# Performance work log

Hardware: AMD Instinct MI355X
Metric: run time of the kernel (lower is better)

Reference implementation:

```python
import jax, jax.numpy as jnp
import numpy as np

B, N1, N2, D, L, H = 2, 384, 384, 128, 3, 128
DM_MIN = 0.5


def _gat_layer(x, adj, W, Wb, A, gW, gb):
    # GAT_gate from jaechanglim/DTI_PDBbind: attention softmax over dim 1, gated residual
    h = x @ W + Wb                                   # [B,N,D]
    e = jnp.einsum('bjl,bkl->bjk', h @ A, h)
    e = e + jnp.swapaxes(e, 1, 2)
    att = jnp.where(adj > 0, e, -9e15)
    att = jax.nn.softmax(att, axis=1) * adj
    h_prime = jax.nn.relu(jnp.einsum('bij,bjk->bik', att, h))
    coeff = jax.nn.sigmoid(jnp.concatenate([x, h_prime], -1) @ gW + gb)  # [B,N,1]
    return coeff * x + (1.0 - coeff) * h_prime


def _pair_mlp(h1g, h2g, W1, b1, W2, b2):
    # MLP(concat(h1_i, h2_j)) without materializing the [B,N1,N2,2D] concat:
    # split W1 into ligand / protein halves and broadcast-add the projections.
    p1 = jnp.einsum('bnd,dk->bnk', h1g, W1[:D])      # [B,N1,H]
    p2 = jnp.einsum('bmd,dk->bmk', h2g, W1[D:])      # [B,N2,H]
    hid = jax.nn.relu(p1[:, :, None, :] + p2[:, None, :, :] + b1)  # [B,N1,N2,H]
    return (hid @ W2 + b2)[..., 0]                   # [B,N1,N2]


def reference(h1, adj1, h2, dmv, charge1, charge2, vdw_epsilon, vdw_sigma,
              delta_uff, valid1, valid2, no_metal1, no_metal2,
              node_W, gat_W, gat_Wb, gat_A, gat_gW, gat_gb,
              pair_W1, pair_b1, pair_W2, pair_b2,
              vdw_coeff, duff_coeff, int_W1, int_b1, int_W2, int_b2):
    h1g = h1 @ node_W
    h2g = h2 @ node_W
    for i in range(L):  # only ligand graph is convolved (as in the source)
        h1g = _gat_layer(h1g, adj1, gat_W[i], gat_Wb[i], gat_A[i], gat_gW[i], gat_gb[i])

    dm = jnp.sqrt(jnp.sum(dmv * dmv, -1) + 1e-10)    # [B,N1,N2]
    dm = jnp.where(dm < DM_MIN, 1e10, dm)

    # coulomb term (pair MLPs 0,1)
    cA = jax.nn.sigmoid(_pair_mlp(h1g, h2g, pair_W1[0], pair_b1[0], pair_W2[0], pair_b2[0]))
    cN = jax.nn.sigmoid(_pair_mlp(h1g, h2g, pair_W1[1], pair_b1[1], pair_W2[1], pair_b2[1])) * 2.0 + 1.0
    charge12 = charge1[:, :, None] * charge2[:, None, :]
    e_c = cA * charge12 * jnp.power(1.0 / dm, cN)
    e_c = e_c * valid1[:, :, None] * valid2[:, None, :]
    e_c = jnp.clip(e_c, -100.0, 100.0)
    e_c = jnp.sum(e_c, axis=(1, 2))[:, None]

    # vdw term (pair MLPs 2=A sigmoid, 3=B tanh, 4=N sigmoid)
    vA = (jax.nn.sigmoid(_pair_mlp(h1g, h2g, pair_W1[2], pair_b1[2], pair_W2[2], pair_b2[2])) * 0.6 + 0.7)
    vA = vA * (vdw_coeff[0] * vdw_coeff[0]) * vdw_epsilon
    vB = jnp.tanh(_pair_mlp(h1g, h2g, pair_W1[3], pair_b1[3], pair_W2[3], pair_b2[3])) * 0.6 + 0.7
    vN = jax.nn.sigmoid(_pair_mlp(h1g, h2g, pair_W1[4], pair_b1[4], pair_W2[4], pair_b2[4])) * 2.0 + 5.0
    dm0 = vdw_sigma * vB
    dm0 = jnp.where(dm0 < 1e-4, 1.0, dm0)
    r = jnp.power(dm0 / dm, vN)
    e_v = vA * (r * r - 2.0 * r)                     # (dm0/dm)^(2N) - 2(dm0/dm)^N
    e_v = e_v * no_metal1[:, :, None] * no_metal2[:, None, :]
    e_v = jnp.minimum(e_v, 100.0)
    e_v = jnp.sum(e_v, axis=(1, 2))[:, None]

    # conformational energy difference term
    e_u = (duff_coeff[0] * duff_coeff[0] * delta_uff)[:, None]

    # learned intercept from pooled ligand features
    hs = jnp.sum(h1g * valid1[..., None], axis=1)
    inter = jax.nn.relu(hs @ int_W1 + int_b1) @ int_W2 + int_b2

    return jnp.concatenate([e_c, e_v, e_u, inter], -1)  # [B,4]


def setup_inputs() -> dict:
    key = jax.random.key(0)
    ks = jax.random.split(key, 24)
    inp = {}
    inp['h1'] = jax.random.normal(ks[0], (B, N1, 54), jnp.float32)
    inp['h2'] = jax.random.normal(ks[1], (B, N2, 54), jnp.float32)
    a = jax.random.uniform(ks[2], (B, N1, N1))
    adj = (a > 0.9).astype(jnp.float32)
    adj = jnp.maximum(adj, jnp.swapaxes(adj, 1, 2))
    inp['adj1'] = jnp.maximum(adj, jnp.eye(N1, dtype=jnp.float32)[None])
    inp['dmv'] = jax.random.normal(ks[3], (B, N1, N2, 3), jnp.float32) * 3.0
    inp['charge1'] = jax.random.normal(ks[4], (B, N1), jnp.float32) * 0.3
    inp['charge2'] = jax.random.normal(ks[5], (B, N2), jnp.float32) * 0.3
    inp['vdw_epsilon'] = jax.random.uniform(ks[6], (B, N1, N2), jnp.float32) * 0.3
    inp['vdw_sigma'] = 3.0 + jax.random.uniform(ks[7], (B, N1, N2), jnp.float32)
    inp['delta_uff'] = jax.random.uniform(ks[8], (B,), jnp.float32) * 5.0
    inp['valid1'] = jnp.ones((B, N1), jnp.float32)
    inp['valid2'] = jnp.ones((B, N2), jnp.float32)
    inp['no_metal1'] = jnp.ones((B, N1), jnp.float32)
    inp['no_metal2'] = jnp.ones((B, N2), jnp.float32)
    # parameters
    inp['node_W'] = jax.random.normal(ks[9], (54, D), jnp.float32) * 0.1
    inp['gat_W'] = jax.random.normal(ks[10], (L, D, D), jnp.float32) * (1.0 / np.sqrt(D))
    inp['gat_Wb'] = jnp.zeros((L, D), jnp.float32)
    inp['gat_A'] = jax.random.normal(ks[11], (L, D, D), jnp.float32) * 0.05
    inp['gat_gW'] = jax.random.normal(ks[12], (L, 2 * D, 1), jnp.float32) * 0.05
    inp['gat_gb'] = jnp.zeros((L, 1), jnp.float32)
    inp['pair_W1'] = jax.random.normal(ks[13], (5, 2 * D, H), jnp.float32) * 0.05
    inp['pair_b1'] = jnp.zeros((5, H), jnp.float32)
    inp['pair_W2'] = jax.random.normal(ks[14], (5, H, 1), jnp.float32) * 0.1
    inp['pair_b2'] = jnp.zeros((5, 1), jnp.float32)
    inp['vdw_coeff'] = jnp.array([0.02], jnp.float32)
    inp['duff_coeff'] = jnp.array([0.1], jnp.float32)
    inp['int_W1'] = jax.random.normal(ks[15], (D, H), jnp.float32) * 0.05
    inp['int_b1'] = jnp.zeros((H,), jnp.float32)
    inp['int_W2'] = jax.random.normal(ks[16], (H, 1), jnp.float32) * 0.1
    inp['int_b2'] = jnp.zeros((1,), jnp.float32)
    return inp
```

## Files before the change

### kernel.cpp

```cpp
#include <hip/hip_runtime.h>
#include <math.h>

#define BB 2
#define NN 384
#define DD 128
#define HH 128
#define RT_ALL (BB * NN)
#define PCOLS (BB * NN)

__device__ __forceinline__ float sigmoidf_(float x) { return 1.f / (1.f + __expf(-x)); }
__device__ __forceinline__ float tanhf_(float x)    { return 1.f - 2.f / (__expf(2.f * x) + 1.f); }

__global__ __launch_bounds__(256) void k_embed(
    const float* __restrict__ h1, const float* __restrict__ h2,
    const float* __restrict__ nW, float* __restrict__ h1g, float* __restrict__ h2g) {
  int r0 = blockIdx.x * 2;
  int tid = threadIdx.x;
  const float* src; float* dst; int rb;
  if (r0 < RT_ALL) { src = h1; dst = h1g; rb = r0; }
  else             { src = h2; dst = h2g; rb = r0 - RT_ALL; }
  __shared__ float xs[2][54];
  if (tid < 108) xs[tid / 54][tid % 54] = src[rb * 54 + tid];
  __syncthreads();
  int rr = tid >> 7, c = tid & 127;
  float acc = 0.f;
#pragma unroll 6
  for (int k = 0; k < 54; ++k) acc += xs[rr][k] * nW[k * DD + c];
  dst[(rb + rr) * DD + c] = acc;
}

__global__ __launch_bounds__(256) void k_gat_hhA(
    const float* __restrict__ x, const float* __restrict__ W,
    const float* __restrict__ Wb, const float* __restrict__ A,
    float* __restrict__ h, float* __restrict__ hA,
    float* __restrict__ hT, float* __restrict__ hAT) {
  int r = blockIdx.x;
  int tid = threadIdx.x, c = tid & 127, kh = tid >> 7;
  __shared__ float xs[DD], hs[DD];
  __shared__ float ph[2][DD];
  if (tid < DD) xs[tid] = x[r * DD + tid];
  __syncthreads();
  float acc = 0.f;
  const float* Wp = W + (kh * 64) * DD + c;
#pragma unroll 4
  for (int k = 0; k < 64; ++k) acc += xs[kh * 64 + k] * Wp[k * DD];
  ph[kh][c] = acc;
  __syncthreads();
  if (tid < DD) {
    float hv = ph[0][tid] + ph[1][tid] + Wb[tid];
    h[r * DD + tid] = hv; hT[tid * PCOLS + r] = hv; hs[tid] = hv;
  }
  __syncthreads();
  acc = 0.f;
  const float* Ap = A + (kh * 64) * DD + c;
#pragma unroll 4
  for (int k = 0; k < 64; ++k) acc += hs[kh * 64 + k] * Ap[k * DD];
  ph[kh][c] = acc;
  __syncthreads();
  if (tid < DD) {
    float av = ph[0][tid] + ph[1][tid];
    hA[r * DD + tid] = av; hAT[tid * PCOLS + r] = av;
  }
}

__global__ __launch_bounds__(384) void k_gat_att(
    const float* __restrict__ h, const float* __restrict__ hA,
    const float* __restrict__ hT, const float* __restrict__ hAT,
    const float* __restrict__ adj, float* __restrict__ att) {
  int col = blockIdx.x;
  int b = col / NN, k = col - b * NN;
  int tid = threadIdx.x;
  __shared__ float hrow_s[DD], hArow_s[DD];
  __shared__ float rmx[6], rsm[6];
  if (tid < DD) hrow_s[tid] = h[col * DD + tid];
  else if (tid < 2 * DD) hArow_s[tid - DD] = hA[col * DD + tid - DD];
  __syncthreads();
  const float* hTb  = hT  + b * NN + tid;
  const float* hATb = hAT + b * NN + tid;
  float e = 0.f;
#pragma unroll 8
  for (int c = 0; c < DD; ++c)
    e += hATb[c * PCOLS] * hrow_s[c] + hTb[c * PCOLS] * hArow_s[c];
  float a = adj[col * NN + tid];
  float lmax = (a > 0.f) ? e : -3e38f;
#pragma unroll
  for (int off = 32; off > 0; off >>= 1) lmax = fmaxf(lmax, __shfl_down(lmax, off));
  if ((tid & 63) == 0) rmx[tid >> 6] = lmax;
  __syncthreads();
  float m = fmaxf(fmaxf(fmaxf(rmx[0], rmx[1]), fmaxf(rmx[2], rmx[3])), fmaxf(rmx[4], rmx[5]));
  float v = (a > 0.f) ? __expf(e - m) : 0.f;
  float s = v;
#pragma unroll
  for (int off = 32; off > 0; off >>= 1) s += __shfl_down(s, off);
  if ((tid & 63) == 0) rsm[tid >> 6] = s;
  __syncthreads();
  float inv = 1.f / (rsm[0] + rsm[1] + rsm[2] + rsm[3] + rsm[4] + rsm[5]);
  att[(b * NN + tid) * NN + k] = v * a * inv;
}

__global__ __launch_bounds__(256) void k_gat_out(
    const float* __restrict__ x, const float* __restrict__ h,
    const float* __restrict__ att, const float* __restrict__ gW,
    const float* __restrict__ gb, float* __restrict__ out) {
  int r = blockIdx.x;
  int b = r / NN;
  int tid = threadIdx.x, c = tid & 127, jh = tid >> 7;
  __shared__ float arow[NN];
  __shared__ float ph[2][DD];
  __shared__ float redw[2];
  if (tid < 96) ((float4*)arow)[tid] = ((const float4*)(att + r * NN))[tid];
  __syncthreads();
  float accA = 0.f, accB = 0.f;
  const float* hp = h + (b * NN + jh * 192) * DD + c;
  const float* ar = arow + jh * 192;
#pragma unroll 4
  for (int jj = 0; jj < 192; jj += 2) {
    accA += ar[jj] * hp[jj * DD];
    accB += ar[jj + 1] * hp[(jj + 1) * DD];
  }
  ph[jh][c] = accA + accB;
  __syncthreads();
  if (tid < DD) {
    float hpr = fmaxf(ph[0][tid] + ph[1][tid], 0.f);
    float xr = x[r * DD + tid];
    float v = xr * gW[tid] + hpr * gW[DD + tid];
#pragma unroll
    for (int off = 32; off > 0; off >>= 1) v += __shfl_down(v, off);
    if ((tid & 63) == 0) redw[tid >> 6] = v;
  }
  __syncthreads();
  if (tid < DD) {
    float hpr = fmaxf(ph[0][tid] + ph[1][tid], 0.f);
    float xr = x[r * DD + tid];
    float coeff = sigmoidf_(redw[0] + redw[1] + gb[0]);
    out[r * DD + tid] = coeff * xr + (1.f - coeff) * hpr;
  }
}

__global__ __launch_bounds__(256) void k_pair_proj(
    const float* __restrict__ h1g, const float* __restrict__ h2g,
    const float* __restrict__ W1, const float* __restrict__ b1,
    const float* __restrict__ delta_uff, const float* __restrict__ duff_coeff,
    float* __restrict__ p1, float* __restrict__ p2q, float* __restrict__ out) {
  const int RT = 16;
  int m = blockIdx.x % 5;
  int r0 = (blockIdx.x / 5) * RT;
  int tid = threadIdx.x, c = tid & 127, kh = tid >> 7;
  if (blockIdx.x == 0 && tid < BB * 4) {
    int bb = tid >> 2, cc = tid & 3;
    out[tid] = (cc == 2) ? duff_coeff[0] * duff_coeff[0] * delta_uff[bb] : 0.f;
  }
  bool lig = (r0 < RT_ALL);
  const float* src = lig ? h1g : h2g;
  int rb = lig ? r0 : r0 - RT_ALL;
  const float* W = W1 + (m * 256 + (lig ? 0 : 128)) * HH;
  __shared__ float xs[RT][DD];
  __shared__ float ps[RT][DD];
  for (int idx = tid; idx < RT * DD; idx += 256) xs[idx >> 7][idx & 127] = src[rb * DD + idx];
  __syncthreads();
  float acc[RT];
#pragma unroll
  for (int r = 0; r < RT; ++r) acc[r] = 0.f;
  const float* Wp = W + (kh * 64) * HH + c;
#pragma unroll 2
  for (int k = 0; k < 64; ++k) {
    float w = Wp[k * HH];
#pragma unroll
    for (int r = 0; r < RT; ++r) acc[r] += xs[r][kh * 64 + k] * w;
  }
  if (kh == 1) {
#pragma unroll
    for (int r = 0; r < RT; ++r) ps[r][c] = acc[r];
  }
  __syncthreads();
  if (kh == 0) {
    if (lig) {
      float bias = b1[m * HH + c];
#pragma unroll
      for (int r = 0; r < RT; ++r)
        p1[((rb + r) * 5 + m) * HH + c] = acc[r] + ps[r][c] + bias;
    } else {
      int g = m * (HH / 4) + (c >> 2);
      float* dst = p2q + (size_t)(g * PCOLS + rb) * 4 + (c & 3);
#pragma unroll
      for (int r = 0; r < RT; ++r) dst[4 * r] = acc[r] + ps[r][c];
    }
  }
}

__global__ __launch_bounds__(192) void k_pair_energy(
    const float* __restrict__ p1, const float* __restrict__ p2q,
    const float* __restrict__ W2, const float* __restrict__ b2,
    const float* __restrict__ dmv, const float* __restrict__ charge1,
    const float* __restrict__ charge2, const float* __restrict__ veps,
    const float* __restrict__ vsig, const float* __restrict__ valid1,
    const float* __restrict__ valid2, const float* __restrict__ nm1,
    const float* __restrict__ nm2, const float* __restrict__ vdw_coeff,
    const float* __restrict__ h1g, float* __restrict__ ws_int,
    float* __restrict__ out) {
  int tid = threadIdx.x;
  if (blockIdx.x >= 768) {
    int eb = blockIdx.x - 768;
    int b = eb >> 2, ch = eb & 3;
    if (tid < DD) {
      float acc = 0.f;
      int i0 = ch * 96;
#pragma unroll 4
      for (int i = 0; i < 96; ++i) {
        int gi = b * NN + i0 + i;
        acc += h1g[gi * DD + tid] * valid1[gi];
      }
      ws_int[eb * DD + tid] = acc;
    }
    return;
  }
  const int TI = 2;
  int tile = blockIdx.x >> 1, jh = blockIdx.x & 1;
  int r0 = tile * TI;
  int b = r0 / NN;
  int j = jh * 192 + tid;
  int col = b * NN + j;

  __shared__ float4 p1s4[2][5 * HH / 4];
  __shared__ float4 w2s4[5 * HH / 4];
  {
    const float4* p1g = (const float4*)(p1 + r0 * 5 * HH);
    for (int idx = tid; idx < 2 * 160; idx += 192) p1s4[idx / 160][idx % 160] = p1g[idx];
    if (tid < 160) w2s4[tid] = ((const float4*)W2)[tid];
  }
  __syncthreads();

  const float4* p2q4 = (const float4*)p2q;
  float acc0[5], acc1[5];
#pragma unroll
  for (int m = 0; m < 5; ++m) {
    const float4* pc = p2q4 + (size_t)(m * 32) * PCOLS + col;
    float a0 = 0.f, a1 = 0.f;
#pragma unroll 8
    for (int hq = 0; hq < 32; ++hq) {
      float4 pv = pc[(size_t)hq * PCOLS];
      float4 x0 = p1s4[0][m * 32 + hq];
      float4 x1 = p1s4[1][m * 32 + hq];
      float4 w  = w2s4[m * 32 + hq];
      a0 += fmaxf(x0.x + pv.x, 0.f) * w.x + fmaxf(x0.y + pv.y, 0.f) * w.y
          + fmaxf(x0.z + pv.z, 0.f) * w.z + fmaxf(x0.w + pv.w, 0.f) * w.w;
      a1 += fmaxf(x1.x + pv.x, 0.f) * w.x + fmaxf(x1.y + pv.y, 0.f) * w.y
          + fmaxf(x1.z + pv.z, 0.f) * w.z + fmaxf(x1.w + pv.w, 0.f) * w.w;
    }
    acc0[m] = a0 + b2[m]; acc1[m] = a1 + b2[m];
  }

  float q2c = charge2[col], v2 = valid2[col], n2 = nm2[col];
  float vc2 = vdw_coeff[0] * vdw_coeff[0];
  float ec_sum = 0.f, ev_sum = 0.f;
#pragma unroll
  for (int ti = 0; ti < TI; ++ti) {
    const float* am = ti ? acc1 : acc0;
    int gi = r0 + ti;
    int pidx = gi * NN + j;
    float dx = dmv[pidx * 3 + 0], dy = dmv[pidx * 3 + 1], dz = dmv[pidx * 3 + 2];
    float dm = sqrtf(dx * dx + dy * dy + dz * dz + 1e-10f);
    if (dm < 0.5f) dm = 1e10f;
    float cA = sigmoidf_(am[0]);
    float cN = sigmoidf_(am[1]) * 2.f + 1.f;
    float e_c = cA * charge1[gi] * q2c * __powf(1.f / dm, cN);
    e_c *= valid1[gi] * v2;
    e_c = fminf(fmaxf(e_c, -100.f), 100.f);
    ec_sum += e_c;
    float vA = (sigmoidf_(am[2]) * 0.6f + 0.7f) * vc2 * veps[pidx];
    float vB = tanhf_(am[3]) * 0.6f + 0.7f;
    float vN = sigmoidf_(am[4]) * 2.f + 5.f;
    float dm0 = vsig[pidx] * vB;
    if (dm0 < 1e-4f) dm0 = 1.f;
    float rr = __powf(dm0 / dm, vN);
    float e_v = vA * (rr * rr - 2.f * rr);
    e_v *= nm1[gi] * n2;
    e_v = fminf(e_v, 100.f);
    ev_sum += e_v;
  }
#pragma unroll
  for (int off = 32; off > 0; off >>= 1) {
    ec_sum += __shfl_down(ec_sum, off);
    ev_sum += __shfl_down(ev_sum, off);
  }
  __shared__ float rec[3], rev[3];
  if ((tid & 63) == 0) { rec[tid >> 6] = ec_sum; rev[tid >> 6] = ev_sum; }
  __syncthreads();
  if (tid == 0) {
    atomicAdd(&out[b * 4 + 0], rec[0] + rec[1] + rec[2]);
    atomicAdd(&out[b * 4 + 1], rev[0] + rev[1] + rev[2]);
  }
}

__global__ __launch_bounds__(256) void k_intercept_fin(
    const float* __restrict__ ws_int, const float* __restrict__ W1,
    const float* __restrict__ b1, const float* __restrict__ W2,
    const float* __restrict__ b2, float* __restrict__ out) {
  int b = blockIdx.x;
  int tid = threadIdx.x, c = tid & 127, kh = tid >> 7;
  __shared__ float hsf[DD];
  __shared__ float ph[2][DD];
  __shared__ float redw[2];
  if (tid < DD)
    hsf[tid] = ws_int[(b * 4 + 0) * DD + tid] + ws_int[(b * 4 + 1) * DD + tid]
             + ws_int[(b * 4 + 2) * DD + tid] + ws_int[(b * 4 + 3) * DD + tid];
  __syncthreads();
  float acc = 0.f;
  const float* Wp = W1 + (kh * 64) * HH + c;
#pragma unroll 4
  for (int k = 0; k < 64; ++k) acc += hsf[kh * 64 + k] * Wp[k * HH];
  ph[kh][c] = acc;
  __syncthreads();
  if (tid < DD) {
    float hid = fmaxf(ph[0][tid] + ph[1][tid] + b1[tid], 0.f);
    float v = hid * W2[tid];
#pragma unroll
    for (int off = 32; off > 0; off >>= 1) v += __shfl_down(v, off);
    if ((tid & 63) == 0) redw[tid >> 6] = v;
  }
  __syncthreads();
  if (tid == 0) out[b * 4 + 3] = redw[0] + redw[1] + b2[0];
}

extern "C" void kernel_launch(void* const* d_in, const int* in_sizes, int n_in,
                              void* d_out, int out_size, void* d_ws, size_t ws_size,
                              hipStream_t stream) {
  (void)in_sizes; (void)n_in; (void)out_size; (void)ws_size;
  const float* h1         = (const float*)d_in[0];
  const float* h2         = (const float*)d_in[1];
  const float* adj1       = (const float*)d_in[2];
  const float* dmv        = (const float*)d_in[3];
  const float* charge1    = (const float*)d_in[4];
  const float* charge2    = (const float*)d_in[5];
  const float* veps       = (const float*)d_in[6];
  const float* vsig       = (const float*)d_in[7];
  const float* delta_uff  = (const float*)d_in[8];
  const float* valid1     = (const float*)d_in[9];
  const float* valid2     = (const float*)d_in[10];
  const float* nm1        = (const float*)d_in[11];
  const float* nm2        = (const float*)d_in[12];
  const float* node_W     = (const float*)d_in[13];
  const float* gat_W      = (const float*)d_in[14];
  const float* gat_Wb     = (const float*)d_in[15];
  const float* gat_A      = (const float*)d_in[16];
  const float* gat_gW     = (const float*)d_in[17];
  const float* gat_gb     = (const float*)d_in[18];
  const float* pW1        = (const float*)d_in[19];
  const float* pb1        = (const float*)d_in[20];
  const float* pW2        = (const float*)d_in[21];
  const float* pb2        = (const float*)d_in[22];
  const float* vdw_coeff  = (const float*)d_in[23];
  const float* duff_coeff = (const float*)d_in[24];
  const float* iW1        = (const float*)d_in[25];
  const float* ib1        = (const float*)d_in[26];
  const float* iW2        = (const float*)d_in[27];
  const float* ib2        = (const float*)d_in[28];
  float* out = (float*)d_out;

  float* ws = (float*)d_ws;
  const int RN = BB * NN * DD;
  float* h1gA   = ws;
  float* h1gB   = h1gA + RN;
  float* h2g    = h1gB + RN;
  float* hbuf   = h2g + RN;
  float* hAbuf  = hbuf + RN;
  float* hTbuf  = hAbuf + RN;
  float* hATbuf = hTbuf + RN;
  float* att    = hATbuf + RN;
  float* p1     = att + BB * NN * NN;
  float* p2q    = p1 + BB * NN * 5 * HH;
  float* ws_int = p2q + 5 * HH * PCOLS;

  k_embed<<<dim3(2 * BB * NN / 2), dim3(256), 0, stream>>>(h1, h2, node_W, h1gA, h2g);

  float* cur = h1gA;
  float* nxt = h1gB;
  for (int l = 0; l < 3; ++l) {
    k_gat_hhA<<<dim3(BB * NN), dim3(256), 0, stream>>>(
        cur, gat_W + l * DD * DD, gat_Wb + l * DD, gat_A + l * DD * DD,
        hbuf, hAbuf, hTbuf, hATbuf);
    k_gat_att<<<dim3(BB * NN), dim3(384), 0, stream>>>(
        hbuf, hAbuf, hTbuf, hATbuf, adj1, att);
    k_gat_out<<<dim3(BB * NN), dim3(256), 0, stream>>>(
        cur, hbuf, att, gat_gW + l * 2 * DD, gat_gb + l, nxt);
    float* t = cur; cur = nxt; nxt = t;
  }
  const float* h1gF = cur;

  k_pair_proj<<<dim3((2 * BB * NN / 16) * 5), dim3(256), 0, stream>>>(
      h1gF, h2g, pW1, pb1, delta_uff, duff_coeff, p1, p2q, out);
  k_pair_energy<<<dim3(768 + 8), dim3(192), 0, stream>>>(
      p1, p2q, pW2, pb2, dmv, charge1, charge2, veps, vsig,
      valid1, valid2, nm1, nm2, vdw_coeff, h1gF, ws_int, out);
  k_intercept_fin<<<dim3(BB), dim3(256), 0, stream>>>(ws_int, iW1, ib1, iW2, ib2, out);
}
```

Before: 316.2 us.

## Process two rows per block in GAT kernels and drop shared-memory staging

The GAT projection, attention and output kernels now each handle two rows or columns per block, so every weight or h load is reused for two outputs and the launch count is halved. Shared-memory staging of inputs is removed in several kernels in favour of direct global reads, which are uniform across the block and so can be served by scalar or broadcast loads. The pair-energy kernel switches to 384-thread blocks covering a full protein row, reading p1 and W2 from global instead of shared memory. This trades fewer blocks, and possibly lower occupancy, for more reuse per load, and relies on the cache to serve the repeated global reads.

```diff
diff --git a/kernel.cpp b/kernel.cpp
--- a/kernel.cpp
+++ b/kernel.cpp
@@ -19,13 +19,11 @@
   const float* src; float* dst; int rb;
   if (r0 < RT_ALL) { src = h1; dst = h1g; rb = r0; }
   else             { src = h2; dst = h2g; rb = r0 - RT_ALL; }
-  __shared__ float xs[2][54];
-  if (tid < 108) xs[tid / 54][tid % 54] = src[rb * 54 + tid];
-  __syncthreads();
   int rr = tid >> 7, c = tid & 127;
+  const float* xr = src + (rb + rr) * 54;
   float acc = 0.f;
 #pragma unroll 6
-  for (int k = 0; k < 54; ++k) acc += xs[rr][k] * nW[k * DD + c];
+  for (int k = 0; k < 54; ++k) acc += xr[k] * nW[k * DD + c];
   dst[(rb + rr) * DD + c] = acc;
 }
 
@@ -34,32 +32,46 @@
     const float* __restrict__ Wb, const float* __restrict__ A,
     float* __restrict__ h, float* __restrict__ hA,
     float* __restrict__ hT, float* __restrict__ hAT) {
-  int r = blockIdx.x;
+  int r0 = blockIdx.x * 2;
   int tid = threadIdx.x, c = tid & 127, kh = tid >> 7;
-  __shared__ float xs[DD], hs[DD];
-  __shared__ float ph[2][DD];
-  if (tid < DD) xs[tid] = x[r * DD + tid];
-  __syncthreads();
-  float acc = 0.f;
+  __shared__ float ph[2][2][DD];
+  __shared__ float hs[2][DD];
+  const float* x0 = x + (r0 + 0) * DD + kh * 64;
+  const float* x1 = x + (r0 + 1) * DD + kh * 64;
   const float* Wp = W + (kh * 64) * DD + c;
-#pragma unroll 4
-  for (int k = 0; k < 64; ++k) acc += xs[kh * 64 + k] * Wp[k * DD];
-  ph[kh][c] = acc;
-  __syncthreads();
-  if (tid < DD) {
-    float hv = ph[0][tid] + ph[1][tid] + Wb[tid];
-    h[r * DD + tid] = hv; hT[tid * PCOLS + r] = hv; hs[tid] = hv;
-  }
-  __syncthreads();
-  acc = 0.f;
+  float a00 = 0.f, a01 = 0.f, a10 = 0.f, a11 = 0.f;
+#pragma unroll 4
+  for (int k = 0; k < 64; k += 2) {
+    float w0 = Wp[k * DD], w1 = Wp[(k + 1) * DD];
+    a00 += x0[k] * w0; a01 += x0[k + 1] * w1;
+    a10 += x1[k] * w0; a11 += x1[k + 1] * w1;
+  }
+  ph[kh][0][c] = a00 + a01;
+  ph[kh][1][c] = a10 + a11;
+  __syncthreads();
+  {
+    float hv = ph[0][kh][c] + ph[1][kh][c] + Wb[c];
+    h[(r0 + kh) * DD + c] = hv;
+    hT[c * PCOLS + r0 + kh] = hv;
+    hs[kh][c] = hv;
+  }
+  __syncthreads();
   const float* Ap = A + (kh * 64) * DD + c;
-#pragma unroll 4
-  for (int k = 0; k < 64; ++k) acc += hs[kh * 64 + k] * Ap[k * DD];
-  ph[kh][c] = acc;
-  __syncthreads();
-  if (tid < DD) {
-    float av = ph[0][tid] + ph[1][tid];
-    hA[r * DD + tid] = av; hAT[tid * PCOLS + r] = av;
+  a00 = a01 = a10 = a11 = 0.f;
+#pragma unroll 4
+  for (int k = 0; k < 64; k += 2) {
+    float w0 = Ap[k * DD], w1 = Ap[(k + 1) * DD];
+    a00 += hs[0][kh * 64 + k] * w0; a01 += hs[0][kh * 64 + k + 1] * w1;
+    a10 += hs[1][kh * 64 + k] * w0; a11 += hs[1][kh * 64 + k + 1] * w1;
+  }
+  __syncthreads();
+  ph[kh][0][c] = a00 + a01;
+  ph[kh][1][c] = a10 + a11;
+  __syncthreads();
+  {
+    float av = ph[0][kh][c] + ph[1][kh][c];
+    hA[(r0 + kh) * DD + c] = av;
+    hAT[c * PCOLS + r0 + kh] = av;
   }
 }
 
@@ -67,74 +79,87 @@
     const float* __restrict__ h, const float* __restrict__ hA,
     const float* __restrict__ hT, const float* __restrict__ hAT,
     const float* __restrict__ adj, float* __restrict__ att) {
-  int col = blockIdx.x;
-  int b = col / NN, k = col - b * NN;
+  int b = blockIdx.x / (NN / 2);
+  int k0 = (blockIdx.x % (NN / 2)) * 2;
+  int col0 = b * NN + k0, col1 = col0 + 1;
   int tid = threadIdx.x;
-  __shared__ float hrow_s[DD], hArow_s[DD];
-  __shared__ float rmx[6], rsm[6];
-  if (tid < DD) hrow_s[tid] = h[col * DD + tid];
-  else if (tid < 2 * DD) hArow_s[tid - DD] = hA[col * DD + tid - DD];
-  __syncthreads();
+  const float* hr0  = h  + col0 * DD;
+  const float* har0 = hA + col0 * DD;
+  const float* hr1  = h  + col1 * DD;
+  const float* har1 = hA + col1 * DD;
   const float* hTb  = hT  + b * NN + tid;
   const float* hATb = hAT + b * NN + tid;
-  float e = 0.f;
-#pragma unroll 8
-  for (int c = 0; c < DD; ++c)
-    e += hATb[c * PCOLS] * hrow_s[c] + hTb[c * PCOLS] * hArow_s[c];
-  float a = adj[col * NN + tid];
-  float lmax = (a > 0.f) ? e : -3e38f;
-#pragma unroll
-  for (int off = 32; off > 0; off >>= 1) lmax = fmaxf(lmax, __shfl_down(lmax, off));
-  if ((tid & 63) == 0) rmx[tid >> 6] = lmax;
-  __syncthreads();
-  float m = fmaxf(fmaxf(fmaxf(rmx[0], rmx[1]), fmaxf(rmx[2], rmx[3])), fmaxf(rmx[4], rmx[5]));
-  float v = (a > 0.f) ? __expf(e - m) : 0.f;
-  float s = v;
-#pragma unroll
-  for (int off = 32; off > 0; off >>= 1) s += __shfl_down(s, off);
-  if ((tid & 63) == 0) rsm[tid >> 6] = s;
-  __syncthreads();
-  float inv = 1.f / (rsm[0] + rsm[1] + rsm[2] + rsm[3] + rsm[4] + rsm[5]);
-  att[(b * NN + tid) * NN + k] = v * a * inv;
+  float e0a = 0.f, e0b = 0.f, e1a = 0.f, e1b = 0.f;
+#pragma unroll 4
+  for (int c = 0; c < DD; ++c) {
+    float hTv = hTb[c * PCOLS], hATv = hATb[c * PCOLS];
+    e0a += hATv * hr0[c]; e0b += hTv * har0[c];
+    e1a += hATv * hr1[c]; e1b += hTv * har1[c];
+  }
+  float e0 = e0a + e0b, e1 = e1a + e1b;
+  float a0 = adj[col0 * NN + tid];
+  float a1 = adj[col1 * NN + tid];
+  __shared__ float rmx0[6], rmx1[6], rsm0[6], rsm1[6];
+  float l0 = (a0 > 0.f) ? e0 : -3e38f;
+  float l1 = (a1 > 0.f) ? e1 : -3e38f;
+#pragma unroll
+  for (int off = 32; off > 0; off >>= 1) {
+    l0 = fmaxf(l0, __shfl_down(l0, off));
+    l1 = fmaxf(l1, __shfl_down(l1, off));
+  }
+  if ((tid & 63) == 0) { rmx0[tid >> 6] = l0; rmx1[tid >> 6] = l1; }
+  __syncthreads();
+  float m0 = rmx0[0], m1 = rmx1[0];
+#pragma unroll
+  for (int w = 1; w < 6; ++w) { m0 = fmaxf(m0, rmx0[w]); m1 = fmaxf(m1, rmx1[w]); }
+  float v0 = (a0 > 0.f) ? __expf(e0 - m0) : 0.f;
+  float v1 = (a1 > 0.f) ? __expf(e1 - m1) : 0.f;
+  float s0 = v0, s1 = v1;
+#pragma unroll
+  for (int off = 32; off > 0; off >>= 1) {
+    s0 += __shfl_down(s0, off);
+    s1 += __shfl_down(s1, off);
+  }
+  if ((tid & 63) == 0) { rsm0[tid >> 6] = s0; rsm1[tid >> 6] = s1; }
+  __syncthreads();
+  float d0 = 0.f, d1 = 0.f;
+#pragma unroll
+  for (int w = 0; w < 6; ++w) { d0 += rsm0[w]; d1 += rsm1[w]; }
+  float2 wv = make_float2(v0 * a0 / d0, v1 * a1 / d1);
+  *(float2*)(att + (b * NN + tid) * NN + k0) = wv;
 }
 
 __global__ __launch_bounds__(256) void k_gat_out(
     const float* __restrict__ x, const float* __restrict__ h,
     const float* __restrict__ att, const float* __restrict__ gW,
     const float* __restrict__ gb, float* __restrict__ out) {
-  int r = blockIdx.x;
-  int b = r / NN;
+  int r0 = blockIdx.x * 2;
+  int b = r0 / NN;
   int tid = threadIdx.x, c = tid & 127, jh = tid >> 7;
-  __shared__ float arow[NN];
-  __shared__ float ph[2][DD];
-  __shared__ float redw[2];
-  if (tid < 96) ((float4*)arow)[tid] = ((const float4*)(att + r * NN))[tid];
-  __syncthreads();
-  float accA = 0.f, accB = 0.f;
+  __shared__ float ph[2][2][DD];
+  __shared__ float redw[2][2];
+  const float* ar0 = att + (r0 + 0) * NN + jh * 192;
+  const float* ar1 = att + (r0 + 1) * NN + jh * 192;
   const float* hp = h + (b * NN + jh * 192) * DD + c;
-  const float* ar = arow + jh * 192;
+  float a0A = 0.f, a0B = 0.f, a1A = 0.f, a1B = 0.f;
 #pragma unroll 4
   for (int jj = 0; jj < 192; jj += 2) {
-    accA += ar[jj] * hp[jj * DD];
-    accB += ar[jj + 1] * hp[(jj + 1) * DD];
-  }
-  ph[jh][c] = accA + accB;
-  __syncthreads();
-  if (tid < DD) {
-    float hpr = fmaxf(ph[0][tid] + ph[1][tid], 0.f);
-    float xr = x[r * DD + tid];
-    float v = xr * gW[tid] + hpr * gW[DD + tid];
-#pragma unroll
-    for (int off = 32; off > 0; off >>= 1) v += __shfl_down(v, off);
-    if ((tid & 63) == 0) redw[tid >> 6] = v;
-  }
-  __syncthreads();
-  if (tid < DD) {
-    float hpr = fmaxf(ph[0][tid] + ph[1][tid], 0.f);
-    float xr = x[r * DD + tid];
-    float coeff = sigmoidf_(redw[0] + redw[1] + gb[0]);
-    out[r * DD + tid] = coeff * xr + (1.f - coeff) * hpr;
-  }
+    float hv0 = hp[jj * DD], hv1 = hp[(jj + 1) * DD];
+    a0A += ar0[jj] * hv0; a0B += ar0[jj + 1] * hv1;
+    a1A += ar1[jj] * hv0; a1B += ar1[jj + 1] * hv1;
+  }
+  ph[jh][0][c] = a0A + a0B;
+  ph[jh][1][c] = a1A + a1B;
+  __syncthreads();
+  float hpr = fmaxf(ph[0][jh][c] + ph[1][jh][c], 0.f);
+  float xr = x[(r0 + jh) * DD + c];
+  float v = xr * gW[c] + hpr * gW[DD + c];
+#pragma unroll
+  for (int off = 32; off > 0; off >>= 1) v += __shfl_down(v, off);
+  if ((tid & 63) == 0) redw[jh][(tid >> 6) & 1] = v;
+  __syncthreads();
+  float coeff = sigmoidf_(redw[jh][0] + redw[jh][1] + gb[0]);
+  out[(r0 + jh) * DD + c] = coeff * xr + (1.f - coeff) * hpr;
 }
 
 __global__ __launch_bounds__(256) void k_pair_proj(
@@ -154,20 +179,18 @@
   const float* src = lig ? h1g : h2g;
   int rb = lig ? r0 : r0 - RT_ALL;
   const float* W = W1 + (m * 256 + (lig ? 0 : 128)) * HH;
-  __shared__ float xs[RT][DD];
-  __shared__ float ps[RT][DD];
-  for (int idx = tid; idx < RT * DD; idx += 256) xs[idx >> 7][idx & 127] = src[rb * DD + idx];
-  __syncthreads();
   float acc[RT];
 #pragma unroll
   for (int r = 0; r < RT; ++r) acc[r] = 0.f;
   const float* Wp = W + (kh * 64) * HH + c;
+  const float* xp = src + rb * DD + kh * 64;
 #pragma unroll 2
   for (int k = 0; k < 64; ++k) {
     float w = Wp[k * HH];
 #pragma unroll
-    for (int r = 0; r < RT; ++r) acc[r] += xs[r][kh * 64 + k] * w;
-  }
+    for (int r = 0; r < RT; ++r) acc[r] += xp[r * DD + k] * w;
+  }
+  __shared__ float ps[RT][DD];
   if (kh == 1) {
 #pragma unroll
     for (int r = 0; r < RT; ++r) ps[r][c] = acc[r];
@@ -188,7 +211,7 @@
   }
 }
 
-__global__ __launch_bounds__(192) void k_pair_energy(
+__global__ __launch_bounds__(384) void k_pair_energy(
     const float* __restrict__ p1, const float* __restrict__ p2q,
     const float* __restrict__ W2, const float* __restrict__ b2,
     const float* __restrict__ dmv, const float* __restrict__ charge1,
@@ -199,8 +222,8 @@
     const float* __restrict__ h1g, float* __restrict__ ws_int,
     float* __restrict__ out) {
   int tid = threadIdx.x;
-  if (blockIdx.x >= 768) {
-    int eb = blockIdx.x - 768;
+  if (blockIdx.x >= 384) {
+    int eb = blockIdx.x - 384;
     int b = eb >> 2, ch = eb & 3;
     if (tid < DD) {
       float acc = 0.f;
@@ -214,38 +237,35 @@
     }
     return;
   }
-  const int TI = 2;
-  int tile = blockIdx.x >> 1, jh = blockIdx.x & 1;
-  int r0 = tile * TI;
+  int r0 = blockIdx.x * 2;
   int b = r0 / NN;
-  int j = jh * 192 + tid;
+  int j = tid;
   int col = b * NN + j;
 
-  __shared__ float4 p1s4[2][5 * HH / 4];
-  __shared__ float4 w2s4[5 * HH / 4];
-  {
-    const float4* p1g = (const float4*)(p1 + r0 * 5 * HH);
-    for (int idx = tid; idx < 2 * 160; idx += 192) p1s4[idx / 160][idx % 160] = p1g[idx];
-    if (tid < 160) w2s4[tid] = ((const float4*)W2)[tid];
-  }
-  __syncthreads();
-
+  const float* q0 = p1 + (r0 + 0) * 5 * HH;
+  const float* q1 = p1 + (r0 + 1) * 5 * HH;
   const float4* p2q4 = (const float4*)p2q;
   float acc0[5], acc1[5];
 #pragma unroll
   for (int m = 0; m < 5; ++m) {
     const float4* pc = p2q4 + (size_t)(m * 32) * PCOLS + col;
+    const float* x0m = q0 + m * HH;
+    const float* x1m = q1 + m * HH;
+    const float* w2m = W2 + m * HH;
     float a0 = 0.f, a1 = 0.f;
 #pragma unroll 8
     for (int hq = 0; hq < 32; ++hq) {
       float4 pv = pc[(size_t)hq * PCOLS];
-      float4 x0 = p1s4[0][m * 32 + hq];
-      float4 x1 = p1s4[1][m * 32 + hq];
-      float4 w  = w2s4[m * 32 + hq];
-      a0 += fmaxf(x0.x + pv.x, 0.f) * w.x + fmaxf(x0.y + pv.y, 0.f) * w.y
-          + fmaxf(x0.z + pv.z, 0.f) * w.z + fmaxf(x0.w + pv.w, 0.f) * w.w;
-      a1 += fmaxf(x1.x + pv.x, 0.f) * w.x + fmaxf(x1.y + pv.y, 0.f) * w.y
-          + fmaxf(x1.z + pv.z, 0.f) * w.z + fmaxf(x1.w + pv.w, 0.f) * w.w;
+      float w0 = w2m[4 * hq + 0], w1 = w2m[4 * hq + 1];
+      float w2v = w2m[4 * hq + 2], w3 = w2m[4 * hq + 3];
+      float x00 = x0m[4 * hq + 0], x01 = x0m[4 * hq + 1];
+      float x02 = x0m[4 * hq + 2], x03 = x0m[4 * hq + 3];
+      float x10 = x1m[4 * hq + 0], x11 = x1m[4 * hq + 1];
+      float x12 = x1m[4 * hq + 2], x13 = x1m[4 * hq + 3];
+      a0 += fmaxf(x00 + pv.x, 0.f) * w0 + fmaxf(x01 + pv.y, 0.f) * w1
+          + fmaxf(x02 + pv.z, 0.f) * w2v + fmaxf(x03 + pv.w, 0.f) * w3;
+      a1 += fmaxf(x10 + pv.x, 0.f) * w0 + fmaxf(x11 + pv.y, 0.f) * w1
+          + fmaxf(x12 + pv.z, 0.f) * w2v + fmaxf(x13 + pv.w, 0.f) * w3;
     }
     acc0[m] = a0 + b2[m]; acc1[m] = a1 + b2[m];
   }
@@ -254,7 +274,7 @@
   float vc2 = vdw_coeff[0] * vdw_coeff[0];
   float ec_sum = 0.f, ev_sum = 0.f;
 #pragma unroll
-  for (int ti = 0; ti < TI; ++ti) {
+  for (int ti = 0; ti < 2; ++ti) {
     const float* am = ti ? acc1 : acc0;
     int gi = r0 + ti;
     int pidx = gi * NN + j;
@@ -283,12 +303,15 @@
     ec_sum += __shfl_down(ec_sum, off);
     ev_sum += __shfl_down(ev_sum, off);
   }
-  __shared__ float rec[3], rev[3];
+  __shared__ float rec[6], rev[6];
   if ((tid & 63) == 0) { rec[tid >> 6] = ec_sum; rev[tid >> 6] = ev_sum; }
   __syncthreads();
   if (tid == 0) {
-    atomicAdd(&out[b * 4 + 0], rec[0] + rec[1] + rec[2]);
-    atomicAdd(&out[b * 4 + 1], rev[0] + rev[1] + rev[2]);
+    float a = 0.f, c = 0.f;
+#pragma unroll
+    for (int w = 0; w < 6; ++w) { a += rec[w]; c += rev[w]; }
+    atomicAdd(&out[b * 4 + 0], a);
+    atomicAdd(&out[b * 4 + 1], c);
   }
 }
 
@@ -376,12 +399,12 @@
   float* cur = h1gA;
   float* nxt = h1gB;
   for (int l = 0; l < 3; ++l) {
-    k_gat_hhA<<<dim3(BB * NN), dim3(256), 0, stream>>>(
+    k_gat_hhA<<<dim3(BB * NN / 2), dim3(256), 0, stream>>>(
         cur, gat_W + l * DD * DD, gat_Wb + l * DD, gat_A + l * DD * DD,
         hbuf, hAbuf, hTbuf, hATbuf);
-    k_gat_att<<<dim3(BB * NN), dim3(384), 0, stream>>>(
+    k_gat_att<<<dim3(BB * NN / 2), dim3(384), 0, stream>>>(
         hbuf, hAbuf, hTbuf, hATbuf, adj1, att);
-    k_gat_out<<<dim3(BB * NN), dim3(256), 0, stream>>>(
+    k_gat_out<<<dim3(BB * NN / 2), dim3(256), 0, stream>>>(
         cur, hbuf, att, gat_gW + l * 2 * DD, gat_gb + l, nxt);
     float* t = cur; cur = nxt; nxt = t;
   }
@@ -389,7 +412,7 @@
 
   k_pair_proj<<<dim3((2 * BB * NN / 16) * 5), dim3(256), 0, stream>>>(
       h1gF, h2g, pW1, pb1, delta_uff, duff_coeff, p1, p2q, out);
-  k_pair_energy<<<dim3(768 + 8), dim3(192), 0, stream>>>(
+  k_pair_energy<<<dim3(384 + 8), dim3(384), 0, stream>>>(
       p1, p2q, pW2, pb2, dmv, charge1, charge2, veps, vsig,
       valid1, valid2, nm1, nm2, vdw_coeff, h1gF, ws_int, out);
   k_intercept_fin<<<dim3(BB), dim3(256), 0, stream>>>(ws_int, iW1, ib1, iW2, ib2, out);
```

Result: faster. 302.1 us (-4.5%).
